# Kernel optimization log

Hardware: AMD Instinct MI355X
Metric: run time of the kernel (lower is better)

Reference implementation:

```python
import jax, jax.numpy as jnp
import numpy as np

GRID_SPACING = 0.5  # tf.constant(0.5)


def _mlp(x, W1, b1, W2, b2, W3, b3):
    # tiny base_model: 3 -> H -> H -> 1, positive output (softplus head)
    h = jnp.tanh(x @ W1 + b1)
    h = jnp.tanh(h @ W2 + b2)
    return jax.nn.softplus(h @ W3 + b3)


def setup_inputs() -> dict:
    key = jax.random.key(0)
    ks = jax.random.split(key, 8)
    nx = ny = nz = 128
    N = nx * ny * nz
    Ns = (nx - 1) * (ny - 1) * (nz - 1)
    B, H = 32768, 128
    DATAX = jax.random.uniform(ks[0], (N, 3), dtype=jnp.float32)
    DATAF = jax.random.uniform(ks[1], (N, 1), dtype=jnp.float32)
    STAGX = jax.random.uniform(ks[2], (Ns, 3), dtype=jnp.float32)
    LAPLF = jax.random.uniform(ks[3], (nx - 2, ny - 2, nz - 2), dtype=jnp.float32)
    center_indices = jax.random.randint(ks[4], (B,), 0, N, dtype=jnp.int32)
    W1 = jax.random.normal(ks[5], (3, H), dtype=jnp.float32) * 0.5
    W2 = jax.random.normal(ks[6], (H, H), dtype=jnp.float32) * (1.0 / np.sqrt(H))
    W3 = jax.random.normal(ks[7], (H, 1), dtype=jnp.float32) * (1.0 / np.sqrt(H))
    return {
        'DATAX': DATAX, 'DATAF': DATAF, 'STAGX': STAGX, 'LAPLF': LAPLF,
        'loss_m_weight': jnp.full((1,), 0.5, dtype=jnp.float32),
        'W1': W1, 'b1': jnp.zeros((H,), jnp.float32),
        'W2': W2, 'b2': jnp.zeros((H,), jnp.float32),
        'W3': W3, 'b3': jnp.zeros((1,), jnp.float32),
        'center_indices': center_indices,
    }


def reference(DATAX, DATAF, STAGX, LAPLF, loss_m_weight,
              W1, b1, W2, b2, W3, b3, center_indices):
    nxm2, nym2, nzm2 = LAPLF.shape
    nx, ny, nz = nxm2 + 2, nym2 + 2, nzm2 + 2
    N = nx * ny * nz
    Ns = (nx - 1) * (ny - 1) * (nz - 1)
    ci = center_indices.astype(jnp.int32)

    # decode flat id (z-major: z*nx*ny + y*nx + x)
    i_z = ci // (nx * ny)
    rem = ci % (nx * ny)
    i_y = rem // nx
    i_x = rem % nx
    valid = ((i_x >= 1) & (i_x < nx - 1) & (i_y >= 1) & (i_y < ny - 1)
             & (i_z >= 1) & (i_z < nz - 1))

    # 8 original-grid corners: dx,dy,dz in {-1,1}, dz fastest (list-comp order)
    off = jnp.array([-1, 1], jnp.int32)
    dd = jnp.stack(jnp.meshgrid(off, off, off, indexing='ij'), -1).reshape(8, 3)
    ox = i_x[:, None] + dd[None, :, 0]
    oy = i_y[:, None] + dd[None, :, 1]
    oz = i_z[:, None] + dd[None, :, 2]
    flat_o = jnp.clip(oz * nx * ny + oy * nx + ox, 0, N - 1)  # [B,8]

    # 8 staggered-grid corners: dx,dy,dz in {-1,0}, flat = x*ny'*nz' + y*nz' + z
    offs = jnp.array([-1, 0], jnp.int32)
    ds = jnp.stack(jnp.meshgrid(offs, offs, offs, indexing='ij'), -1).reshape(8, 3)
    sx = i_x[:, None] + ds[None, :, 0]
    sy = i_y[:, None] + ds[None, :, 1]
    sz = i_z[:, None] + ds[None, :, 2]
    flat_s = jnp.clip(sx * (ny - 1) * (nz - 1) + sy * (nz - 1) + sz, 0, Ns - 1)

    fo = _mlp(DATAX[flat_o], W1, b1, W2, b2, W3, b3)[..., 0]  # [B,8]
    fs = _mlp(STAGX[flat_s], W1, b1, W2, b2, W3, b3)[..., 0]  # [B,8]

    # diagonals of the [2,2,2] cube: (000,111),(010,101),(001,110),(011,100)
    ia = jnp.array([0, 2, 1, 3])
    ib = jnp.array([7, 5, 6, 4])
    num = jnp.abs(fo[:, ia] + fo[:, ib] - fs[:, ia] - fs[:, ib])
    den = fo[:, ia] + fo[:, ib] + fs[:, ia] + fs[:, ib]
    delta = 3.0 * (GRID_SPACING ** 2)
    lap = jnp.sum(num / den, axis=1) / (3.0 * delta)  # [B]

    flat_l = jnp.clip((i_x - 1) * nym2 * nzm2 + (i_y - 1) * nzm2 + (i_z - 1),
                      0, nxm2 * nym2 * nzm2 - 1)
    dlap = LAPLF.reshape(-1)[flat_l] - lap
    m = valid.astype(dlap.dtype)
    loss_m = loss_m_weight[0] * (jnp.sum(jnp.square(dlap) * m)
                                 / jnp.maximum(jnp.sum(m), 1.0))

    pred = _mlp(DATAX[ci], W1, b1, W2, b2, W3, b3)[:, 0]
    loss_e = jnp.mean(jnp.abs(pred - DATAF[ci][:, 0]))
    return loss_e + loss_m
```

## Files before the change

### kernel.cpp

```cpp
#include <hip/hip_runtime.h>
#include <stdint.h>

#define NXC   128
#define NXY   16384
#define NTOT  2097152
#define NS    2048383
#define SXY   16129
#define SYC   127
#define LXY   15876
#define LTOT  2000376

#define SCALE 2.8853900817779268f

typedef __bf16 bf16x8 __attribute__((ext_vector_type(8)));
typedef float f32x4 __attribute__((ext_vector_type(4)));
typedef float f32x2 __attribute__((ext_vector_type(2)));

typedef const __attribute__((address_space(1))) uint32_t* gas_t;
typedef __attribute__((address_space(3))) uint32_t* las_t;

__device__ __forceinline__ float rcp_hw(float x) {
#if __has_builtin(__builtin_amdgcn_rcpf)
  return __builtin_amdgcn_rcpf(x);
#else
  return 1.0f / x;
#endif
}
__device__ __forceinline__ float exp2_hw(float x) {
#if __has_builtin(__builtin_amdgcn_exp2f)
  return __builtin_amdgcn_exp2f(x);
#else
  return __exp2f(x);
#endif
}

__device__ __forceinline__ f32x2 tanh_pre2(f32x2 z) {
  f32x2 e;
  e.x = exp2_hw(z.x);
  e.y = exp2_hw(z.y);
  f32x2 ep1 = e + 1.0f;
  f32x2 r;
  r.x = rcp_hw(ep1.x);
  r.y = rcp_hw(ep1.y);
  return 1.0f - 2.0f * r;
}

__device__ __forceinline__ float softplus_f(float x) {
  float a = fabsf(x);
  return fmaxf(x, 0.0f) + __logf(1.0f + __expf(-a));
}

__device__ __forceinline__ void ld8v(const float* p, f32x2* o) {
  float4 a = *reinterpret_cast<const float4*>(p);
  float4 b = *reinterpret_cast<const float4*>(p + 4);
  o[0].x = a.x; o[0].y = a.y;
  o[1].x = a.z; o[1].y = a.w;
  o[2].x = b.x; o[2].y = b.y;
  o[3].x = b.z; o[3].y = b.w;
}

__global__ __launch_bounds__(256) void conv_kernel(
    const float* __restrict__ W1, const float* __restrict__ B1,
    const float* __restrict__ W2, const float* __restrict__ B2,
    const float* __restrict__ W3,
    __bf16* __restrict__ w2pre, float* __restrict__ smallpre)
{
  const int n = blockIdx.x * 256 + threadIdx.x;
  if (n < 2048) {
    const int c = n >> 7, j = n & 127;
    bf16x8 v;
    #pragma unroll
    for (int e = 0; e < 8; ++e) v[e] = (__bf16)(SCALE * W2[(8 * c + e) * 128 + j]);
    *reinterpret_cast<bf16x8*>(&w2pre[(j << 7) + (((c ^ (j & 15)) & 15) << 3)]) = v;
  }
  if (blockIdx.x == 0) {
    for (int i = threadIdx.x; i < 768; i += 256) {
      float v;
      if (i < 384)      v = SCALE * W1[i];
      else if (i < 512) v = SCALE * B1[i - 384];
      else {
        int q = (i - 512) >> 1;
        v = ((i & 1) == 0) ? (SCALE * B2[q]) : W3[q];
      }
      smallpre[i] = v;
    }
  }
}

__global__ __launch_bounds__(256) void mlp_kernel(
    const float* __restrict__ DATAX, const float* __restrict__ STAGX,
    const int* __restrict__ CI,
    const __bf16* __restrict__ w2pre, const float* __restrict__ smallpre,
    const float* __restrict__ B3, float* __restrict__ fout)
{
  __shared__ __align__(16) __bf16 w2t[16384];

  const int tid  = threadIdx.x;
  const int lane = tid & 63;
  const int wid  = tid >> 6;
  const int cl   = lane & 15;
  const int g    = lane >> 4;

  const int group = (blockIdx.x << 2) + wid;
  const int gbase = group << 6;
  const int p = gbase + lane;
  const unsigned bb = (unsigned)p / 17u;
  const int t = p - (int)bb * 17;
  const int ci = CI[bb];

  {
    const char* gsrc = (const char*)w2pre + (wid << 13) + (lane << 4);
    char*       ldst = (char*)w2t + (wid << 13);
    #pragma unroll
    for (int i = 0; i < 8; ++i) {
      __builtin_amdgcn_global_load_lds(
          (gas_t)(const void*)(gsrc + (i << 10)),
          (las_t)(void*)(ldst + (i << 10)), 16, 0, 0);
    }
  }

  const int iz = ci >> 14, rem = ci & 16383, iy = rem >> 7, ix = rem & 127;
  const float* xp;
  if (t < 8) {
    int ox = ix + ((t & 4) ? 1 : -1);
    int oy = iy + ((t & 2) ? 1 : -1);
    int oz = iz + ((t & 1) ? 1 : -1);
    int fl = oz * NXY + oy * NXC + ox;
    fl = min(max(fl, 0), NTOT - 1);
    xp = DATAX + 3 * fl;
  } else if (t < 16) {
    int ts = t - 8;
    int sx = ix + ((ts & 4) ? 0 : -1);
    int sy = iy + ((ts & 2) ? 0 : -1);
    int sz = iz + ((ts & 1) ? 0 : -1);
    int fl = sx * SXY + sy * SYC + sz;
    fl = min(max(fl, 0), NS - 1);
    xp = STAGX + 3 * fl;
  } else {
    xp = DATAX + 3 * ci;
  }
  const float px = xp[0], py = xp[1], pz = xp[2];
  const float b3v = B3[0];

  const float* w1s = smallpre;
  const float* b1s = smallpre + 384;
  const float* bw  = smallpre + 512;

  __syncthreads();

  float rxv[4], ryv[4], rzv[4];
  #pragma unroll
  for (int mt = 0; mt < 4; ++mt) {
    int src = (mt << 4) + cl;
    rxv[mt] = __shfl(px, src);
    ryv[mt] = __shfl(py, src);
    rzv[mt] = __shfl(pz, src);
  }

  bf16x8 A[4][4];
  #pragma unroll
  for (int kt = 0; kt < 4; ++kt) {
    int k0 = (kt << 5) + (g << 3);
    f32x2 wx2[4], wy2[4], wz2[4], bv2[4];
    ld8v(&w1s[k0], wx2);
    ld8v(&w1s[128 + k0], wy2);
    ld8v(&w1s[256 + k0], wz2);
    ld8v(&b1s[k0], bv2);
    #pragma unroll
    for (int mt = 0; mt < 4; ++mt) {
      #pragma unroll
      for (int i = 0; i < 4; ++i) {
        f32x2 pre = rxv[mt] * wx2[i] + ryv[mt] * wy2[i]
                  + rzv[mt] * wz2[i] + bv2[i];
        f32x2 th = tanh_pre2(pre);
        A[mt][kt][2 * i]     = (__bf16)th.x;
        A[mt][kt][2 * i + 1] = (__bf16)th.y;
      }
    }
  }

  f32x2 s2[4][2];
  #pragma unroll
  for (int mt = 0; mt < 4; ++mt) {
    s2[mt][0] = 0.0f;
    s2[mt][1] = 0.0f;
  }

  #pragma unroll
  for (int nt = 0; nt < 8; ++nt) {
    const float2 bwv = *reinterpret_cast<const float2*>(&bw[(cl + (nt << 4)) << 1]);
    const float b2v = bwv.x, w3v = bwv.y;
    f32x4 cc[4];
    #pragma unroll
    for (int mt = 0; mt < 4; ++mt) {
      f32x4 seed = {b2v, b2v, b2v, b2v};
      cc[mt] = seed;
    }
    const int row = (nt << 4) + cl;
    #pragma unroll
    for (int kt = 0; kt < 4; ++kt) {
      int chunk = (kt << 2) + g;
      bf16x8 bfv = *reinterpret_cast<const bf16x8*>(
          &w2t[(row << 7) + ((chunk ^ cl) << 3)]);
      #pragma unroll
      for (int mt = 0; mt < 4; ++mt)
        cc[mt] = __builtin_amdgcn_mfma_f32_16x16x32_bf16(A[mt][kt], bfv, cc[mt], 0, 0, 0);
    }
    #pragma unroll
    for (int mt = 0; mt < 4; ++mt) {
      f32x2 lo, hi;
      lo.x = cc[mt][0]; lo.y = cc[mt][1];
      hi.x = cc[mt][2]; hi.y = cc[mt][3];
      s2[mt][0] += tanh_pre2(lo) * w3v;
      s2[mt][1] += tanh_pre2(hi) * w3v;
    }
  }

  float s[4][4];
  #pragma unroll
  for (int mt = 0; mt < 4; ++mt) {
    s[mt][0] = s2[mt][0].x; s[mt][1] = s2[mt][0].y;
    s[mt][2] = s2[mt][1].x; s[mt][3] = s2[mt][1].y;
    #pragma unroll
    for (int r = 0; r < 4; ++r) {
      float v = s[mt][r];
      v += __shfl_xor(v, 1);
      v += __shfl_xor(v, 2);
      v += __shfl_xor(v, 4);
      v += __shfl_xor(v, 8);
      s[mt][r] = v;
    }
  }
  if (cl == 0) {
    #pragma unroll
    for (int mt = 0; mt < 4; ++mt) {
      int base = gbase + (mt << 4) + (g << 2);
      float4 o;
      o.x = softplus_f(s[mt][0] + b3v);
      o.y = softplus_f(s[mt][1] + b3v);
      o.z = softplus_f(s[mt][2] + b3v);
      o.w = softplus_f(s[mt][3] + b3v);
      *reinterpret_cast<float4*>(&fout[base]) = o;
    }
  }
}

__global__ __launch_bounds__(256) void reduce1(
    const float* __restrict__ f, const int* __restrict__ CI,
    const float* __restrict__ LAPLF, const float* __restrict__ DATAF,
    float* __restrict__ partials, int B)
{
  const int tid = threadIdx.x;
  const int b = blockIdx.x * 256 + tid;
  float sq = 0.f, mv = 0.f, ae = 0.f;
  if (b < B) {
    int ci = CI[b];
    int iz = ci >> 14, rem = ci & 16383, iy = rem >> 7, ix = rem & 127;
    bool valid = (ix >= 1) & (ix < 127) & (iy >= 1) & (iy < 127) &
                 (iz >= 1) & (iz < 127);
    const float* fb = f + b * 17;
    float fo[8], fs[8];
    #pragma unroll
    for (int i = 0; i < 8; ++i) { fo[i] = fb[i]; fs[i] = fb[8 + i]; }
    float pred = fb[16];
    const int ia[4] = {0, 2, 1, 3};
    const int ib[4] = {7, 5, 6, 4};
    float lap = 0.f;
    #pragma unroll
    for (int r = 0; r < 4; ++r) {
      float aa = fo[ia[r]] + fo[ib[r]];
      float bs = fs[ia[r]] + fs[ib[r]];
      lap += fabsf(aa - bs) / (aa + bs);
    }
    lap *= (1.0f / 2.25f);
    int fl = (ix - 1) * LXY + (iy - 1) * 126 + (iz - 1);
    fl = min(max(fl, 0), LTOT - 1);
    float dlap = LAPLF[fl] - lap;
    if (valid) { sq = dlap * dlap; mv = 1.f; }
    ae = fabsf(pred - DATAF[ci]);
  }
  #pragma unroll
  for (int msk = 32; msk >= 1; msk >>= 1) {
    sq += __shfl_xor(sq, msk);
    mv += __shfl_xor(mv, msk);
    ae += __shfl_xor(ae, msk);
  }
  __shared__ float rs[3][4];
  int lane = tid & 63, wd = tid >> 6;
  if (lane == 0) { rs[0][wd] = sq; rs[1][wd] = mv; rs[2][wd] = ae; }
  __syncthreads();
  if (tid == 0) {
    partials[blockIdx.x * 3 + 0] = rs[0][0] + rs[0][1] + rs[0][2] + rs[0][3];
    partials[blockIdx.x * 3 + 1] = rs[1][0] + rs[1][1] + rs[1][2] + rs[1][3];
    partials[blockIdx.x * 3 + 2] = rs[2][0] + rs[2][1] + rs[2][2] + rs[2][3];
  }
}

__global__ __launch_bounds__(128) void reduce2(
    const float* __restrict__ partials, const float* __restrict__ lw,
    float* __restrict__ out, int np, float invB)
{
  const int t = threadIdx.x;
  float sq = 0.f, mv = 0.f, ae = 0.f;
  for (int i = t; i < np; i += 128) {
    sq += partials[3 * i + 0];
    mv += partials[3 * i + 1];
    ae += partials[3 * i + 2];
  }
  #pragma unroll
  for (int msk = 32; msk >= 1; msk >>= 1) {
    sq += __shfl_xor(sq, msk);
    mv += __shfl_xor(mv, msk);
    ae += __shfl_xor(ae, msk);
  }
  __shared__ float rs[3][2];
  int lane = t & 63, wd = t >> 6;
  if (lane == 0) { rs[0][wd] = sq; rs[1][wd] = mv; rs[2][wd] = ae; }
  __syncthreads();
  if (t == 0) {
    float S = rs[0][0] + rs[0][1];
    float M = rs[1][0] + rs[1][1];
    float A = rs[2][0] + rs[2][1];
    out[0] = lw[0] * (S / fmaxf(M, 1.0f)) + A * invB;
  }
}

extern "C" void kernel_launch(void* const* d_in, const int* in_sizes, int n_in,
                              void* d_out, int out_size, void* d_ws, size_t ws_size,
                              hipStream_t stream) {
  const float* DATAX = (const float*)d_in[0];
  const float* DATAF = (const float*)d_in[1];
  const float* STAGX = (const float*)d_in[2];
  const float* LAPLF = (const float*)d_in[3];
  const float* LW    = (const float*)d_in[4];
  const float* W1    = (const float*)d_in[5];
  const float* B1    = (const float*)d_in[6];
  const float* W2    = (const float*)d_in[7];
  const float* B2    = (const float*)d_in[8];
  const float* W3    = (const float*)d_in[9];
  const float* B3    = (const float*)d_in[10];
  const int*   CI    = (const int*)d_in[11];

  const int B = in_sizes[11];
  const int P = 17 * B;
  const int ngroups = P >> 6;
  const int nblocks = ngroups >> 2;

  __bf16* w2pre    = (__bf16*)d_ws;
  float*  smallpre = (float*)((char*)d_ws + 32768);
  float*  fbuf     = (float*)((char*)d_ws + 36864);
  float*  partials = fbuf + P;

  conv_kernel<<<8, 256, 0, stream>>>(W1, B1, W2, B2, W3, w2pre, smallpre);
  mlp_kernel<<<nblocks, 256, 0, stream>>>(DATAX, STAGX, CI, w2pre, smallpre,
                                          B3, fbuf);
  const int nb2 = (B + 255) >> 8;
  reduce1<<<nb2, 256, 0, stream>>>(fbuf, CI, LAPLF, DATAF, partials, B);
  reduce2<<<1, 128, 0, stream>>>(partials, LW, (float*)d_out, nb2, 1.0f / (float)B);
}
```

Before: 64.52 us.

## Process two 64-point groups per wave to amortize W2 LDS staging

Each wave now handles 128 points, two groups of 64, instead of 64, which halves the number of blocks. The gathers for both groups are issued up front so their latency overlaps the W2 global-to-LDS copy. A sched_barrier separates the two group iterations to keep register pressure in check. The goal is to spread the per-block cost of loading 32KB of W2 into LDS over twice as much work, at the price of fewer blocks in flight and a longer serial run per wave.

```diff
diff --git a/kernel.cpp b/kernel.cpp
--- a/kernel.cpp
+++ b/kernel.cpp
@@ -57,6 +57,32 @@
   o[1].x = a.z; o[1].y = a.w;
   o[2].x = b.x; o[2].y = b.y;
   o[3].x = b.z; o[3].y = b.w;
+}
+
+__device__ __forceinline__ const float* point_addr(
+    int p, const float* __restrict__ DATAX, const float* __restrict__ STAGX,
+    const int* __restrict__ CI) {
+  const unsigned bb = (unsigned)p / 17u;
+  const int t = p - (int)bb * 17;
+  const int ci = CI[bb];
+  const int iz = ci >> 14, rem = ci & 16383, iy = rem >> 7, ix = rem & 127;
+  if (t < 8) {
+    int ox = ix + ((t & 4) ? 1 : -1);
+    int oy = iy + ((t & 2) ? 1 : -1);
+    int oz = iz + ((t & 1) ? 1 : -1);
+    int fl = oz * NXY + oy * NXC + ox;
+    fl = min(max(fl, 0), NTOT - 1);
+    return DATAX + 3 * fl;
+  } else if (t < 16) {
+    int ts = t - 8;
+    int sx = ix + ((ts & 4) ? 0 : -1);
+    int sy = iy + ((ts & 2) ? 0 : -1);
+    int sz = iz + ((ts & 1) ? 0 : -1);
+    int fl = sx * SXY + sy * SYC + sz;
+    fl = min(max(fl, 0), NS - 1);
+    return STAGX + 3 * fl;
+  }
+  return DATAX + 3 * ci;
 }
 
 __global__ __launch_bounds__(256) void conv_kernel(
@@ -101,12 +127,17 @@
   const int cl   = lane & 15;
   const int g    = lane >> 4;
 
-  const int group = (blockIdx.x << 2) + wid;
-  const int gbase = group << 6;
-  const int p = gbase + lane;
-  const unsigned bb = (unsigned)p / 17u;
-  const int t = p - (int)bb * 17;
-  const int ci = CI[bb];
+  const int wgrp  = (blockIdx.x << 2) + wid;
+  const int gbase = wgrp << 7;
+  const int pA = gbase + lane;
+  const int pB = pA + 64;
+
+  const float* xpA = point_addr(pA, DATAX, STAGX, CI);
+  const float* xpB = point_addr(pB, DATAX, STAGX, CI);
+  float pxg[2], pyg[2], pzg[2];
+  pxg[0] = xpA[0]; pyg[0] = xpA[1]; pzg[0] = xpA[2];
+  pxg[1] = xpB[0]; pyg[1] = xpB[1]; pzg[1] = xpB[2];
+  const float b3v = B3[0];
 
   {
     const char* gsrc = (const char*)w2pre + (wid << 13) + (lane << 4);
@@ -119,129 +150,108 @@
     }
   }
 
-  const int iz = ci >> 14, rem = ci & 16383, iy = rem >> 7, ix = rem & 127;
-  const float* xp;
-  if (t < 8) {
-    int ox = ix + ((t & 4) ? 1 : -1);
-    int oy = iy + ((t & 2) ? 1 : -1);
-    int oz = iz + ((t & 1) ? 1 : -1);
-    int fl = oz * NXY + oy * NXC + ox;
-    fl = min(max(fl, 0), NTOT - 1);
-    xp = DATAX + 3 * fl;
-  } else if (t < 16) {
-    int ts = t - 8;
-    int sx = ix + ((ts & 4) ? 0 : -1);
-    int sy = iy + ((ts & 2) ? 0 : -1);
-    int sz = iz + ((ts & 1) ? 0 : -1);
-    int fl = sx * SXY + sy * SYC + sz;
-    fl = min(max(fl, 0), NS - 1);
-    xp = STAGX + 3 * fl;
-  } else {
-    xp = DATAX + 3 * ci;
-  }
-  const float px = xp[0], py = xp[1], pz = xp[2];
-  const float b3v = B3[0];
-
   const float* w1s = smallpre;
   const float* b1s = smallpre + 384;
   const float* bw  = smallpre + 512;
 
   __syncthreads();
 
-  float rxv[4], ryv[4], rzv[4];
   #pragma unroll
-  for (int mt = 0; mt < 4; ++mt) {
-    int src = (mt << 4) + cl;
-    rxv[mt] = __shfl(px, src);
-    ryv[mt] = __shfl(py, src);
-    rzv[mt] = __shfl(pz, src);
-  }
-
-  bf16x8 A[4][4];
-  #pragma unroll
-  for (int kt = 0; kt < 4; ++kt) {
-    int k0 = (kt << 5) + (g << 3);
-    f32x2 wx2[4], wy2[4], wz2[4], bv2[4];
-    ld8v(&w1s[k0], wx2);
-    ld8v(&w1s[128 + k0], wy2);
-    ld8v(&w1s[256 + k0], wz2);
-    ld8v(&b1s[k0], bv2);
+  for (int gi = 0; gi < 2; ++gi) {
+    const float px = pxg[gi], py = pyg[gi], pz = pzg[gi];
+
+    float rxv[4], ryv[4], rzv[4];
     #pragma unroll
     for (int mt = 0; mt < 4; ++mt) {
-      #pragma unroll
-      for (int i = 0; i < 4; ++i) {
-        f32x2 pre = rxv[mt] * wx2[i] + ryv[mt] * wy2[i]
-                  + rzv[mt] * wz2[i] + bv2[i];
-        f32x2 th = tanh_pre2(pre);
-        A[mt][kt][2 * i]     = (__bf16)th.x;
-        A[mt][kt][2 * i + 1] = (__bf16)th.y;
-      }
-    }
-  }
-
-  f32x2 s2[4][2];
-  #pragma unroll
-  for (int mt = 0; mt < 4; ++mt) {
-    s2[mt][0] = 0.0f;
-    s2[mt][1] = 0.0f;
-  }
-
-  #pragma unroll
-  for (int nt = 0; nt < 8; ++nt) {
-    const float2 bwv = *reinterpret_cast<const float2*>(&bw[(cl + (nt << 4)) << 1]);
-    const float b2v = bwv.x, w3v = bwv.y;
-    f32x4 cc[4];
+      int src = (mt << 4) + cl;
+      rxv[mt] = __shfl(px, src);
+      ryv[mt] = __shfl(py, src);
+      rzv[mt] = __shfl(pz, src);
+    }
+
+    bf16x8 A[4][4];
+    #pragma unroll
+    for (int kt = 0; kt < 4; ++kt) {
+      int k0 = (kt << 5) + (g << 3);
+      f32x2 wx2[4], wy2[4], wz2[4], bv2[4];
+      ld8v(&w1s[k0], wx2);
+      ld8v(&w1s[128 + k0], wy2);
+      ld8v(&w1s[256 + k0], wz2);
+      ld8v(&b1s[k0], bv2);
+      #pragma unroll
+      for (int mt = 0; mt < 4; ++mt) {
+        #pragma unroll
+        for (int i = 0; i < 4; ++i) {
+          f32x2 pre = rxv[mt] * wx2[i] + ryv[mt] * wy2[i]
+                    + rzv[mt] * wz2[i] + bv2[i];
+          f32x2 th = tanh_pre2(pre);
+          A[mt][kt][2 * i]     = (__bf16)th.x;
+          A[mt][kt][2 * i + 1] = (__bf16)th.y;
+        }
+      }
+    }
+
+    f32x2 s2[4][2];
     #pragma unroll
     for (int mt = 0; mt < 4; ++mt) {
-      f32x4 seed = {b2v, b2v, b2v, b2v};
-      cc[mt] = seed;
-    }
-    const int row = (nt << 4) + cl;
-    #pragma unroll
-    for (int kt = 0; kt < 4; ++kt) {
-      int chunk = (kt << 2) + g;
-      bf16x8 bfv = *reinterpret_cast<const bf16x8*>(
-          &w2t[(row << 7) + ((chunk ^ cl) << 3)]);
-      #pragma unroll
-      for (int mt = 0; mt < 4; ++mt)
-        cc[mt] = __builtin_amdgcn_mfma_f32_16x16x32_bf16(A[mt][kt], bfv, cc[mt], 0, 0, 0);
-    }
+      s2[mt][0] = 0.0f;
+      s2[mt][1] = 0.0f;
+    }
+
+    #pragma unroll
+    for (int nt = 0; nt < 8; ++nt) {
+      const float2 bwv = *reinterpret_cast<const float2*>(&bw[(cl + (nt << 4)) << 1]);
+      const float b2v = bwv.x, w3v = bwv.y;
+      f32x4 cc[4];
+      #pragma unroll
+      for (int mt = 0; mt < 4; ++mt) {
+        f32x4 seed = {b2v, b2v, b2v, b2v};
+        cc[mt] = seed;
+      }
+      const int row = (nt << 4) + cl;
+      #pragma unroll
+      for (int kt = 0; kt < 4; ++kt) {
+        int chunk = (kt << 2) + g;
+        bf16x8 bfv = *reinterpret_cast<const bf16x8*>(
+            &w2t[(row << 7) + ((chunk ^ cl) << 3)]);
+        #pragma unroll
+        for (int mt = 0; mt < 4; ++mt)
+          cc[mt] = __builtin_amdgcn_mfma_f32_16x16x32_bf16(A[mt][kt], bfv, cc[mt], 0, 0, 0);
+      }
+      #pragma unroll
+      for (int mt = 0; mt < 4; ++mt) {
+        f32x2 lo, hi;
+        lo.x = cc[mt][0]; lo.y = cc[mt][1];
+        hi.x = cc[mt][2]; hi.y = cc[mt][3];
+        s2[mt][0] += tanh_pre2(lo) * w3v;
+        s2[mt][1] += tanh_pre2(hi) * w3v;
+      }
+    }
+
     #pragma unroll
     for (int mt = 0; mt < 4; ++mt) {
-      f32x2 lo, hi;
-      lo.x = cc[mt][0]; lo.y = cc[mt][1];
-      hi.x = cc[mt][2]; hi.y = cc[mt][3];
-      s2[mt][0] += tanh_pre2(lo) * w3v;
-      s2[mt][1] += tanh_pre2(hi) * w3v;
-    }
-  }
-
-  float s[4][4];
-  #pragma unroll
-  for (int mt = 0; mt < 4; ++mt) {
-    s[mt][0] = s2[mt][0].x; s[mt][1] = s2[mt][0].y;
-    s[mt][2] = s2[mt][1].x; s[mt][3] = s2[mt][1].y;
-    #pragma unroll
-    for (int r = 0; r < 4; ++r) {
-      float v = s[mt][r];
-      v += __shfl_xor(v, 1);
-      v += __shfl_xor(v, 2);
-      v += __shfl_xor(v, 4);
-      v += __shfl_xor(v, 8);
-      s[mt][r] = v;
-    }
-  }
-  if (cl == 0) {
-    #pragma unroll
-    for (int mt = 0; mt < 4; ++mt) {
-      int base = gbase + (mt << 4) + (g << 2);
-      float4 o;
-      o.x = softplus_f(s[mt][0] + b3v);
-      o.y = softplus_f(s[mt][1] + b3v);
-      o.z = softplus_f(s[mt][2] + b3v);
-      o.w = softplus_f(s[mt][3] + b3v);
-      *reinterpret_cast<float4*>(&fout[base]) = o;
-    }
+      float s[4] = {s2[mt][0].x, s2[mt][0].y, s2[mt][1].x, s2[mt][1].y};
+      #pragma unroll
+      for (int r = 0; r < 4; ++r) {
+        float v = s[r];
+        v += __shfl_xor(v, 1);
+        v += __shfl_xor(v, 2);
+        v += __shfl_xor(v, 4);
+        v += __shfl_xor(v, 8);
+        s[r] = v;
+      }
+      if (cl == 0) {
+        int base = gbase + (gi << 6) + (mt << 4) + (g << 2);
+        float4 o;
+        o.x = softplus_f(s[0] + b3v);
+        o.y = softplus_f(s[1] + b3v);
+        o.z = softplus_f(s[2] + b3v);
+        o.w = softplus_f(s[3] + b3v);
+        *reinterpret_cast<float4*>(&fout[base]) = o;
+      }
+    }
+
+    __builtin_amdgcn_sched_barrier(0);
   }
 }
 
@@ -343,8 +353,8 @@
 
   const int B = in_sizes[11];
   const int P = 17 * B;
-  const int ngroups = P >> 6;
-  const int nblocks = ngroups >> 2;
+  const int nwaves = P >> 7;
+  const int nblocks = nwaves >> 2;
 
   __bf16* w2pre    = (__bf16*)d_ws;
   float*  smallpre = (float*)((char*)d_ws + 32768);
```

After: 73.34 us. 13.7% more time.

## Read W2 from global memory directly, drop LDS staging and use one-wave blocks

Applied to the files above, without the earlier changes.

The MLP kernel no longer stages the 32 KB bf16 W2 matrix into shared memory with a block-wide barrier. Each wave now reads its B fragments straight from global memory, relying on L1/L2 caching, and blocks shrink to a single 64-thread wave with no __syncthreads. The conversion kernel writes W2 transposed without the XOR swizzle and uses 64 blocks. This removes the LDS fill and barrier cost and the LDS occupancy limit, at the price of repeated global and cache reads of W2 inside the MFMA loop.

```diff
diff --git a/kernel.cpp b/kernel.cpp
--- a/kernel.cpp
+++ b/kernel.cpp
@@ -15,9 +15,6 @@
 typedef __bf16 bf16x8 __attribute__((ext_vector_type(8)));
 typedef float f32x4 __attribute__((ext_vector_type(4)));
 typedef float f32x2 __attribute__((ext_vector_type(2)));
-
-typedef const __attribute__((address_space(1))) uint32_t* gas_t;
-typedef __attribute__((address_space(3))) uint32_t* las_t;
 
 __device__ __forceinline__ float rcp_hw(float x) {
 #if __has_builtin(__builtin_amdgcn_rcpf)
@@ -66,58 +63,38 @@
     __bf16* __restrict__ w2pre, float* __restrict__ smallpre)
 {
   const int n = blockIdx.x * 256 + threadIdx.x;
-  if (n < 2048) {
-    const int c = n >> 7, j = n & 127;
-    bf16x8 v;
-    #pragma unroll
-    for (int e = 0; e < 8; ++e) v[e] = (__bf16)(SCALE * W2[(8 * c + e) * 128 + j]);
-    *reinterpret_cast<bf16x8*>(&w2pre[(j << 7) + (((c ^ (j & 15)) & 15) << 3)]) = v;
-  }
-  if (blockIdx.x == 0) {
-    for (int i = threadIdx.x; i < 768; i += 256) {
-      float v;
-      if (i < 384)      v = SCALE * W1[i];
-      else if (i < 512) v = SCALE * B1[i - 384];
-      else {
-        int q = (i - 512) >> 1;
-        v = ((i & 1) == 0) ? (SCALE * B2[q]) : W3[q];
-      }
-      smallpre[i] = v;
-    }
-  }
-}
-
-__global__ __launch_bounds__(256) void mlp_kernel(
+  if (n < 16384) {
+    const int j = n >> 7, k = n & 127;
+    w2pre[n] = (__bf16)(SCALE * W2[k * 128 + j]);
+  }
+  if (n < 768) {
+    float v;
+    if (n < 384)      v = SCALE * W1[n];
+    else if (n < 512) v = SCALE * B1[n - 384];
+    else {
+      int q = (n - 512) >> 1;
+      v = ((n & 1) == 0) ? (SCALE * B2[q]) : W3[q];
+    }
+    smallpre[n] = v;
+  }
+}
+
+__global__ __launch_bounds__(64) void mlp_kernel(
     const float* __restrict__ DATAX, const float* __restrict__ STAGX,
     const int* __restrict__ CI,
     const __bf16* __restrict__ w2pre, const float* __restrict__ smallpre,
     const float* __restrict__ B3, float* __restrict__ fout)
 {
-  __shared__ __align__(16) __bf16 w2t[16384];
-
-  const int tid  = threadIdx.x;
-  const int lane = tid & 63;
-  const int wid  = tid >> 6;
+  const int lane = threadIdx.x & 63;
   const int cl   = lane & 15;
   const int g    = lane >> 4;
 
-  const int group = (blockIdx.x << 2) + wid;
+  const int group = blockIdx.x;
   const int gbase = group << 6;
   const int p = gbase + lane;
   const unsigned bb = (unsigned)p / 17u;
   const int t = p - (int)bb * 17;
   const int ci = CI[bb];
-
-  {
-    const char* gsrc = (const char*)w2pre + (wid << 13) + (lane << 4);
-    char*       ldst = (char*)w2t + (wid << 13);
-    #pragma unroll
-    for (int i = 0; i < 8; ++i) {
-      __builtin_amdgcn_global_load_lds(
-          (gas_t)(const void*)(gsrc + (i << 10)),
-          (las_t)(void*)(ldst + (i << 10)), 16, 0, 0);
-    }
-  }
 
   const int iz = ci >> 14, rem = ci & 16383, iy = rem >> 7, ix = rem & 127;
   const float* xp;
@@ -146,8 +123,6 @@
   const float* b1s = smallpre + 384;
   const float* bw  = smallpre + 512;
 
-  __syncthreads();
-
   float rxv[4], ryv[4], rzv[4];
   #pragma unroll
   for (int mt = 0; mt < 4; ++mt) {
@@ -199,9 +174,9 @@
     const int row = (nt << 4) + cl;
     #pragma unroll
     for (int kt = 0; kt < 4; ++kt) {
-      int chunk = (kt << 2) + g;
+      const int chunk = (kt << 2) + g;
       bf16x8 bfv = *reinterpret_cast<const bf16x8*>(
-          &w2t[(row << 7) + ((chunk ^ cl) << 3)]);
+          &w2pre[(row << 7) + (chunk << 3)]);
       #pragma unroll
       for (int mt = 0; mt < 4; ++mt)
         cc[mt] = __builtin_amdgcn_mfma_f32_16x16x32_bf16(A[mt][kt], bfv, cc[mt], 0, 0, 0);
@@ -216,30 +191,25 @@
     }
   }
 
-  float s[4][4];
   #pragma unroll
   for (int mt = 0; mt < 4; ++mt) {
-    s[mt][0] = s2[mt][0].x; s[mt][1] = s2[mt][0].y;
-    s[mt][2] = s2[mt][1].x; s[mt][3] = s2[mt][1].y;
+    float s[4] = {s2[mt][0].x, s2[mt][0].y, s2[mt][1].x, s2[mt][1].y};
     #pragma unroll
     for (int r = 0; r < 4; ++r) {
-      float v = s[mt][r];
+      float v = s[r];
       v += __shfl_xor(v, 1);
       v += __shfl_xor(v, 2);
       v += __shfl_xor(v, 4);
       v += __shfl_xor(v, 8);
-      s[mt][r] = v;
-    }
-  }
-  if (cl == 0) {
-    #pragma unroll
-    for (int mt = 0; mt < 4; ++mt) {
+      s[r] = v;
+    }
+    if (cl == 0) {
       int base = gbase + (mt << 4) + (g << 2);
       float4 o;
-      o.x = softplus_f(s[mt][0] + b3v);
-      o.y = softplus_f(s[mt][1] + b3v);
-      o.z = softplus_f(s[mt][2] + b3v);
-      o.w = softplus_f(s[mt][3] + b3v);
+      o.x = softplus_f(s[0] + b3v);
+      o.y = softplus_f(s[1] + b3v);
+      o.z = softplus_f(s[2] + b3v);
+      o.w = softplus_f(s[3] + b3v);
       *reinterpret_cast<float4*>(&fout[base]) = o;
     }
   }
@@ -344,16 +314,15 @@
   const int B = in_sizes[11];
   const int P = 17 * B;
   const int ngroups = P >> 6;
-  const int nblocks = ngroups >> 2;
 
   __bf16* w2pre    = (__bf16*)d_ws;
   float*  smallpre = (float*)((char*)d_ws + 32768);
   float*  fbuf     = (float*)((char*)d_ws + 36864);
   float*  partials = fbuf + P;
 
-  conv_kernel<<<8, 256, 0, stream>>>(W1, B1, W2, B2, W3, w2pre, smallpre);
-  mlp_kernel<<<nblocks, 256, 0, stream>>>(DATAX, STAGX, CI, w2pre, smallpre,
-                                          B3, fbuf);
+  conv_kernel<<<64, 256, 0, stream>>>(W1, B1, W2, B2, W3, w2pre, smallpre);
+  mlp_kernel<<<ngroups, 64, 0, stream>>>(DATAX, STAGX, CI, w2pre, smallpre,
+                                         B3, fbuf);
   const int nb2 = (B + 255) >> 8;
   reduce1<<<nb2, 256, 0, stream>>>(fbuf, CI, LAPLF, DATAF, partials, B);
   reduce2<<<1, 128, 0, stream>>>(partials, LW, (float*)d_out, nb2, 1.0f / (float)B);
```

New measurement: 100.2 us. 55.3% more time.
